# Kernel tuning notes

Hardware: AMD Instinct MI355X
Metric: run time of the kernel (lower is better)

The kernel has to match this reference:

```python
import jax, jax.numpy as jnp
import numpy as np

SIGMA_MAX = 25.0

def marginal_prob_std(t):
    # VE-SDE std: sqrt((sigma_max^(2t) - 1) / (2 ln sigma_max))
    log_s = jnp.log(SIGMA_MAX)
    return jnp.sqrt((jnp.exp(2.0 * t * log_s) - 1.0) / (2.0 * log_s))

def setup_inputs() -> dict:
    key = jax.random.key(0)
    k1, k2, k3 = jax.random.split(key, 3)
    B, N, d = 16384, 16384, 1
    x = jax.random.normal(k1, (B, d), dtype=jnp.float32)
    t = jax.random.uniform(k2, (B,), dtype=jnp.float32, minval=1e-3, maxval=1.0)
    train_data = jax.random.normal(k3, (N, d), dtype=jnp.float32)
    return {"x": x, "t": t, "train_data": train_data}

def reference(x, t, train_data):
    # x: [B,1], t: [B], train_data: [N,1]
    sigma = marginal_prob_std(t)                       # [B]
    sigma2 = sigma * sigma                             # [B]
    # pairwise squared distance (d=1): [N, B]
    diff = train_data - x[:, 0][None, :]               # [N,1]-[1,B] -> broadcast fails; do explicit
    diff = train_data[:, 0][:, None] - x[:, 0][None, :]  # [N, B]
    pdf = jnp.exp(-0.5 * (diff * diff) / sigma2[None, :])  # [N, B]
    num = jnp.sum(pdf * train_data, axis=0)            # [N,B]*[N,1] -> [B]
    den = jnp.sum(pdf, axis=0)                         # [B]
    den_safe = jnp.where(den == 0.0, 1.0, den)
    evals = jnp.where(den == 0.0, 0.0, num / den_safe) # nan -> 0 as in torch code
    evals = evals[:, None]                             # [B,1]
    return (evals - x) / sigma2[:, None]
```

## Files before the change

kernel.cpp:

```cpp
#include <hip/hip_runtime.h>
#include <math.h>


typedef float v2f __attribute__((ext_vector_type(2)));

#define BLK   256
#define CH    512

#if __has_builtin(__builtin_amdgcn_exp2f)
#define EXP2(x) __builtin_amdgcn_exp2f(x)
#else
#define EXP2(x) exp2f(x)
#endif

__device__ __forceinline__ float sigma2_of(float tj) {
  const float TWO_LOG_S = 6.4377516497364011f;
  return (__expf(TWO_LOG_S * tj) - 1.0f) / TWO_LOG_S;
}

template <bool ATOMIC>
__launch_bounds__(BLK)
__global__ void gmm_partial(const float* __restrict__ x,
                            const float* __restrict__ t,
                            const float* __restrict__ td,
                            float* __restrict__ ws,
                            int N, int B) {
  __shared__ float lds[CH];
  const int tid  = threadIdx.x;
  const int j    = blockIdx.x * BLK + tid;
  const int s    = blockIdx.y;
  const int S    = gridDim.y;
  const int base = s * CH;

  for (int i = tid; i < CH; i += BLK) {
    int gi = base + i;
    lds[i] = (gi < N) ? td[gi] : 1e30f;
  }

  float r = 0.0f, y = 0.0f;
  if (j < B) {
    const float HALF_LOG2E = 0.72134752044448170f;
    float s2 = sigma2_of(t[j]);
    r = __fsqrt_rn(HALF_LOG2E / s2);
    y = x[j] * r;
  }
  __syncthreads();

  const v2f rv  = {r, r};
  const v2f nyv = {-y, -y};
  v2f num0 = {0.f, 0.f}, num1 = {0.f, 0.f}, num2 = {0.f, 0.f}, num3 = {0.f, 0.f};
  v2f den0 = {0.f, 0.f}, den1 = {0.f, 0.f}, den2 = {0.f, 0.f}, den3 = {0.f, 0.f};

  const float4* l4 = (const float4*)lds;
  const int iters = CH >> 3;
  #pragma unroll 2
  for (int i = 0; i < iters; ++i) {
    float4 v0 = l4[2 * i];
    float4 v1 = l4[2 * i + 1];
    v2f va = {v0.x, v0.y}, vb = {v0.z, v0.w};
    v2f vc = {v1.x, v1.y}, vd = {v1.z, v1.w};
    v2f da = __builtin_elementwise_fma(va, rv, nyv);
    v2f db = __builtin_elementwise_fma(vb, rv, nyv);
    v2f dc = __builtin_elementwise_fma(vc, rv, nyv);
    v2f dd = __builtin_elementwise_fma(vd, rv, nyv);
    v2f qa = da * da;
    v2f qb = db * db;
    v2f qc = dc * dc;
    v2f qd = dd * dd;
    v2f pa, pb, pc, pd;
    pa.x = EXP2(-qa.x); pa.y = EXP2(-qa.y);
    pb.x = EXP2(-qb.x); pb.y = EXP2(-qb.y);
    pc.x = EXP2(-qc.x); pc.y = EXP2(-qc.y);
    pd.x = EXP2(-qd.x); pd.y = EXP2(-qd.y);
    den0 += pa;
    den1 += pb;
    den2 += pc;
    den3 += pd;
    num0 = __builtin_elementwise_fma(pa, va, num0);
    num1 = __builtin_elementwise_fma(pb, vb, num1);
    num2 = __builtin_elementwise_fma(pc, vc, num2);
    num3 = __builtin_elementwise_fma(pd, vd, num3);
  }
  v2f numv = (num0 + num1) + (num2 + num3);
  v2f denv = (den0 + den1) + (den2 + den3);
  float num = numv.x + numv.y;
  float den = denv.x + denv.y;

  if (j < B) {
    if (ATOMIC) {
      atomicAdd(&ws[j], num);
      atomicAdd(&ws[B + j], den);
    } else {
      ws[(size_t)s * B + j]       = num;
      ws[(size_t)(S + s) * B + j] = den;
    }
  }
}

__global__ void gmm_final(const float* __restrict__ x,
                          const float* __restrict__ t,
                          const float* __restrict__ ws,
                          float* __restrict__ out, int B, int S) {
  int j = blockIdx.x * blockDim.x + threadIdx.x;
  if (j >= B) return;
  float num = 0.f, den = 0.f;
  for (int s = 0; s < S; ++s) {
    num += ws[(size_t)s * B + j];
    den += ws[(size_t)(S + s) * B + j];
  }
  float sigma2 = sigma2_of(t[j]);
  float evals = (den == 0.0f) ? 0.0f : (num / den);
  out[j] = (evals - x[j]) / sigma2;
}

__global__ void zero_kernel(float* __restrict__ p, int n) {
  int i = blockIdx.x * blockDim.x + threadIdx.x;
  if (i < n) p[i] = 0.0f;
}

extern "C" void kernel_launch(void* const* d_in, const int* in_sizes, int n_in,
                              void* d_out, int out_size, void* d_ws, size_t ws_size,
                              hipStream_t stream) {
  const float* x  = (const float*)d_in[0];
  const float* t  = (const float*)d_in[1];
  const float* td = (const float*)d_in[2];
  float* out = (float*)d_out;
  float* ws  = (float*)d_ws;

  const int B = in_sizes[0];
  const int N = in_sizes[2];

  const int S = (N + CH - 1) / CH;
  size_t need = (size_t)2 * S * B * sizeof(float);

  if (ws_size >= need) {
    dim3 grid((B + BLK - 1) / BLK, S);
    gmm_partial<false><<<grid, BLK, 0, stream>>>(x, t, td, ws, N, B);
    gmm_final<<<(B + BLK - 1) / BLK, BLK, 0, stream>>>(x, t, ws, out, B, S);
  } else {
    int nzero = 2 * B;
    zero_kernel<<<(nzero + 255) / 256, 256, 0, stream>>>(ws, nzero);
    dim3 grid((B + BLK - 1) / BLK, S);
    gmm_partial<true><<<grid, BLK, 0, stream>>>(x, t, td, ws, N, B);
    gmm_final<<<(B + BLK - 1) / BLK, BLK, 0, stream>>>(x, t, ws, out, B, 1);
  }
}
```

Baseline: 100.4 us.

## Compute two query points per thread and read training chunk directly from global

Each thread now evaluates two query columns, reusing every loaded training value across both, and the shared-memory staging plus barrier are removed in favour of wave-uniform vector loads from global memory. The training chunk per block is halved, which doubles the number of partial sums written to the workspace and reduced in the final kernel. The aim is to cut load and synchronisation overhead per exponential, at the cost of more workspace traffic and higher register pressure.

After: 109.7 us. 9.3% more time.

```diff
diff --git a/kernel.cpp b/kernel.cpp
--- a/kernel.cpp
+++ b/kernel.cpp
@@ -3,9 +3,11 @@
 
 
 typedef float v2f __attribute__((ext_vector_type(2)));
+typedef float v8f __attribute__((ext_vector_type(8)));
 
-#define BLK   256
-#define CH    512
+#define BLK 256
+#define CH  256
+#define JPB (2 * BLK)
 
 #if __has_builtin(__builtin_amdgcn_exp2f)
 #define EXP2(x) __builtin_amdgcn_exp2f(x)
@@ -25,74 +27,85 @@
                             const float* __restrict__ td,
                             float* __restrict__ ws,
                             int N, int B) {
-  __shared__ float lds[CH];
   const int tid  = threadIdx.x;
-  const int j    = blockIdx.x * BLK + tid;
+  const int j0   = blockIdx.x * JPB + tid;
+  const int j1   = j0 + BLK;
   const int s    = blockIdx.y;
   const int S    = gridDim.y;
   const int base = s * CH;
+  const float* __restrict__ tp = td + base;
+  const int lim = (N - base < CH) ? (N - base) : CH;
 
-  for (int i = tid; i < CH; i += BLK) {
-    int gi = base + i;
-    lds[i] = (gi < N) ? td[gi] : 1e30f;
+  const float HALF_LOG2E = 0.72134752044448170f;
+  float r0 = 0.f, y0 = 0.f, r1 = 0.f, y1 = 0.f;
+  if (j0 < B) { r0 = __fsqrt_rn(HALF_LOG2E / sigma2_of(t[j0])); y0 = x[j0] * r0; }
+  if (j1 < B) { r1 = __fsqrt_rn(HALF_LOG2E / sigma2_of(t[j1])); y1 = x[j1] * r1; }
+
+  const v2f rv0 = {r0, r0}, ny0 = {-y0, -y0};
+  const v2f rv1 = {r1, r1}, ny1 = {-y1, -y1};
+
+  v2f nA0 = {0,0}, nB0 = {0,0}, dA0 = {0,0}, dB0 = {0,0};
+  v2f nA1 = {0,0}, nB1 = {0,0}, dA1 = {0,0}, dB1 = {0,0};
+
+  auto body = [&](v2f g, const v2f& rv, const v2f& ny, v2f& nacc, v2f& dacc) {
+    v2f d = __builtin_elementwise_fma(g, rv, ny);
+    v2f q = d * d;
+    v2f p;
+    p.x = EXP2(-q.x);
+    p.y = EXP2(-q.y);
+    dacc += p;
+    nacc = __builtin_elementwise_fma(p, g, nacc);
+  };
+
+  if (lim == CH) {
+    #pragma unroll 2
+    for (int i = 0; i < CH; i += 8) {
+      v8f f = *(const v8f*)(tp + i);
+      v2f g0 = {f[0], f[1]}, g1 = {f[2], f[3]};
+      v2f g2 = {f[4], f[5]}, g3 = {f[6], f[7]};
+      body(g0, rv0, ny0, nA0, dA0);
+      body(g1, rv0, ny0, nB0, dB0);
+      body(g2, rv0, ny0, nA0, dA0);
+      body(g3, rv0, ny0, nB0, dB0);
+      body(g0, rv1, ny1, nA1, dA1);
+      body(g1, rv1, ny1, nB1, dB1);
+      body(g2, rv1, ny1, nA1, dA1);
+      body(g3, rv1, ny1, nB1, dB1);
+    }
+  } else {
+    for (int i = 0; i < CH; i += 8) {
+      v8f f;
+      #pragma unroll
+      for (int k = 0; k < 8; ++k) f[k] = (i + k < lim) ? tp[i + k] : 1e30f;
+      v2f g0 = {f[0], f[1]}, g1 = {f[2], f[3]};
+      v2f g2 = {f[4], f[5]}, g3 = {f[6], f[7]};
+      body(g0, rv0, ny0, nA0, dA0);
+      body(g1, rv0, ny0, nB0, dB0);
+      body(g2, rv0, ny0, nA0, dA0);
+      body(g3, rv0, ny0, nB0, dB0);
+      body(g0, rv1, ny1, nA1, dA1);
+      body(g1, rv1, ny1, nB1, dB1);
+      body(g2, rv1, ny1, nA1, dA1);
+      body(g3, rv1, ny1, nB1, dB1);
+    }
   }
 
-  float r = 0.0f, y = 0.0f;
-  if (j < B) {
-    const float HALF_LOG2E = 0.72134752044448170f;
-    float s2 = sigma2_of(t[j]);
-    r = __fsqrt_rn(HALF_LOG2E / s2);
-    y = x[j] * r;
-  }
-  __syncthreads();
+  v2f nv0 = nA0 + nB0, dv0 = dA0 + dB0;
+  v2f nv1 = nA1 + nB1, dv1 = dA1 + dB1;
+  float num0 = nv0.x + nv0.y, den0 = dv0.x + dv0.y;
+  float num1 = nv1.x + nv1.y, den1 = dv1.x + dv1.y;
 
-  const v2f rv  = {r, r};
-  const v2f nyv = {-y, -y};
-  v2f num0 = {0.f, 0.f}, num1 = {0.f, 0.f}, num2 = {0.f, 0.f}, num3 = {0.f, 0.f};
-  v2f den0 = {0.f, 0.f}, den1 = {0.f, 0.f}, den2 = {0.f, 0.f}, den3 = {0.f, 0.f};
-
-  const float4* l4 = (const float4*)lds;
-  const int iters = CH >> 3;
-  #pragma unroll 2
-  for (int i = 0; i < iters; ++i) {
-    float4 v0 = l4[2 * i];
-    float4 v1 = l4[2 * i + 1];
-    v2f va = {v0.x, v0.y}, vb = {v0.z, v0.w};
-    v2f vc = {v1.x, v1.y}, vd = {v1.z, v1.w};
-    v2f da = __builtin_elementwise_fma(va, rv, nyv);
-    v2f db = __builtin_elementwise_fma(vb, rv, nyv);
-    v2f dc = __builtin_elementwise_fma(vc, rv, nyv);
-    v2f dd = __builtin_elementwise_fma(vd, rv, nyv);
-    v2f qa = da * da;
-    v2f qb = db * db;
-    v2f qc = dc * dc;
-    v2f qd = dd * dd;
-    v2f pa, pb, pc, pd;
-    pa.x = EXP2(-qa.x); pa.y = EXP2(-qa.y);
-    pb.x = EXP2(-qb.x); pb.y = EXP2(-qb.y);
-    pc.x = EXP2(-qc.x); pc.y = EXP2(-qc.y);
-    pd.x = EXP2(-qd.x); pd.y = EXP2(-qd.y);
-    den0 += pa;
-    den1 += pb;
-    den2 += pc;
-    den3 += pd;
-    num0 = __builtin_elementwise_fma(pa, va, num0);
-    num1 = __builtin_elementwise_fma(pb, vb, num1);
-    num2 = __builtin_elementwise_fma(pc, vc, num2);
-    num3 = __builtin_elementwise_fma(pd, vd, num3);
-  }
-  v2f numv = (num0 + num1) + (num2 + num3);
-  v2f denv = (den0 + den1) + (den2 + den3);
-  float num = numv.x + numv.y;
-  float den = denv.x + denv.y;
-
-  if (j < B) {
-    if (ATOMIC) {
-      atomicAdd(&ws[j], num);
-      atomicAdd(&ws[B + j], den);
-    } else {
-      ws[(size_t)s * B + j]       = num;
-      ws[(size_t)(S + s) * B + j] = den;
+  if (ATOMIC) {
+    if (j0 < B) { atomicAdd(&ws[j0], num0); atomicAdd(&ws[B + j0], den0); }
+    if (j1 < B) { atomicAdd(&ws[j1], num1); atomicAdd(&ws[B + j1], den1); }
+  } else {
+    if (j0 < B) {
+      ws[(size_t)s * B + j0]       = num0;
+      ws[(size_t)(S + s) * B + j0] = den0;
+    }
+    if (j1 < B) {
+      ws[(size_t)s * B + j1]       = num1;
+      ws[(size_t)(S + s) * B + j1] = den1;
     }
   }
 }
@@ -134,13 +147,13 @@
   size_t need = (size_t)2 * S * B * sizeof(float);
 
   if (ws_size >= need) {
-    dim3 grid((B + BLK - 1) / BLK, S);
+    dim3 grid((B + JPB - 1) / JPB, S);
     gmm_partial<false><<<grid, BLK, 0, stream>>>(x, t, td, ws, N, B);
     gmm_final<<<(B + BLK - 1) / BLK, BLK, 0, stream>>>(x, t, ws, out, B, S);
   } else {
     int nzero = 2 * B;
     zero_kernel<<<(nzero + 255) / 256, 256, 0, stream>>>(ws, nzero);
-    dim3 grid((B + BLK - 1) / BLK, S);
+    dim3 grid((B + JPB - 1) / JPB, S);
     gmm_partial<true><<<grid, BLK, 0, stream>>>(x, t, td, ws, N, B);
     gmm_final<<<(B + BLK - 1) / BLK, BLK, 0, stream>>>(x, t, ws, out, B, 1);
   }
```
